# Kernel optimization log

Measured on AMD Instinct MI355X. Metric: run time of the kernel, lower is better.

The kernel has to match this reference:

```python
import jax, jax.numpy as jnp
import numpy as np

N, P, D, LM, NQ = 128, 576, 1536, 4096, 64
ALPHA, FPQ, TEMP, LR_G, EPS = 0.5, 14, 0.5, 0.1, 1e-20
NUM_CUBES = max(round(N / FPQ) - 1, 1)  # static: 8


def setup_inputs() -> dict:
    key = jax.random.key(0)
    ks = jax.random.split(key, 10)
    s = 1.0 / np.sqrt(D)
    return {
        "video_features": jax.random.normal(ks[0], (N, P, D), jnp.float32),
        "gumbel_u": jax.random.uniform(ks[1], (N - 1, 2), jnp.float32),
        "W_agg": jax.random.normal(ks[2], (D, D), jnp.float32) * s,
        "b_agg": jnp.zeros((D,), jnp.float32),
        "ln_g": jnp.ones((D,), jnp.float32),
        "ln_b": jnp.zeros((D,), jnp.float32),
        "W1": jax.random.normal(ks[3], (D, D), jnp.float32) * s,
        "b1": jnp.zeros((D,), jnp.float32),
        "W2": jax.random.normal(ks[4], (D, 2), jnp.float32) * s,
        "b2": jnp.zeros((2,), jnp.float32),
        "W_th": jax.random.normal(ks[5], (D, LM), jnp.float32) * s,
        "b_th": jnp.zeros((LM,), jnp.float32),
    }


def _forward(video_features, gumbel_u, W_agg, b_agg, ln_g, ln_b, W1, b1, W2, b2, W_th, b_th):
    # Step 1: momentum EMA over frame diffs: delta_1 = d_1; delta_i = a*d_i + (1-a)*delta_{i-1}
    diffs = video_features[1:] - video_features[:-1]            # [N-1, P, D]
    def step(carry, d):
        new = ALPHA * d + (1.0 - ALPHA) * carry
        return new, new
    _, rest = jax.lax.scan(step, diffs[0], diffs[1:])
    mom = jnp.concatenate([diffs[:1], rest], axis=0)            # [N-1, P, D]
    # Step 2: aggregate momentum features, mean over patches
    agg = jnp.einsum('npd,de->npe', mom, W_agg) + b_agg
    feat = agg.mean(axis=1)                                     # [N-1, D]
    # Step 3: gate network (LayerNorm -> Linear -> GELU -> Linear)
    mu = feat.mean(-1, keepdims=True)
    var = ((feat - mu) ** 2).mean(-1, keepdims=True)
    xn = (feat - mu) / jnp.sqrt(var + 1e-5) * ln_g + ln_b
    h = jax.nn.gelu(xn @ W1 + b1, approximate=False)
    gate_logits = h @ W2 + b2                                   # [N-1, 2]
    # Step 4: straight-through Gumbel-Softmax top-k
    g = -jnp.log(-jnp.log(gumbel_u + EPS) + EPS)
    y = jax.nn.softmax((gate_logits + g * LR_G) / TEMP, axis=-1)[:, 1]  # [N-1]
    _, ind = jax.lax.top_k(y, NUM_CUBES)
    y_hard = jnp.zeros_like(y).at[ind].set(1.0)
    z_hard = jax.lax.stop_gradient(y_hard - y) + y
    # Step 5: force first frame as keyframe
    z_hard = jnp.concatenate([jnp.ones((1,), z_hard.dtype), z_hard], axis=0)  # [N]
    # Step 7: thumbnail = keyframe-weighted mean -> adaptive avg pool (576->64) -> Linear
    tf = jnp.einsum('n,npd->pd', z_hard, video_features) / z_hard.sum()  # [P, D]
    pooled = tf.reshape(NQ, P // NQ, D).mean(axis=1)                     # [NQ, D]
    thumbnail = pooled @ W_th + b_th                                     # [NQ, LM]
    return gate_logits, thumbnail, z_hard


def reference(video_features, gumbel_u, W_agg, b_agg, ln_g, ln_b, W1, b1, W2, b2, W_th, b_th):
    return _forward(video_features, gumbel_u, W_agg, b_agg, ln_g, ln_b, W1, b1, W2, b2, W_th, b_th)
```

## Files before the change

### kernel.cpp

```cpp
#include <hip/hip_runtime.h>

#define NFR   128
#define PP    576
#define DD    1536
#define LMM   4096
#define NQQ   64
#define PQ    9
#define NCUBES 8
#define NSEL  9
#define D4    384

#define OFF_A      0u
#define OFF_VFMEAN 1572864u
#define OFF_MOM    1769472u
#define OFF_XN     1966080u
#define OFF_H      2162688u
#define OFF_PPART  2359296u
#define OFF_POOLED 3244032u
#define OFF_Y      3342336u
#define OFF_SEL    3342464u

#define OUT_GATE  0
#define OUT_THUMB 254
#define OUT_Z     262398

__global__ __launch_bounds__(384) void k1_partial(const float* __restrict__ vf,
                                                  float* __restrict__ part) {
    const int n  = blockIdx.x;
    const int ps = blockIdx.y;
    const int c4 = threadIdx.x;
    const float4* v = (const float4*)vf;
    float4 acc = make_float4(0.f, 0.f, 0.f, 0.f);
    int base = (n * PP + ps * 72) * D4 + c4;
#pragma unroll 8
    for (int p = 0; p < 72; ++p) {
        float4 x = v[base + p * D4];
        acc.x += x.x; acc.y += x.y; acc.z += x.z; acc.w += x.w;
    }
    ((float4*)part)[(n * 8 + ps) * D4 + c4] = acc;
}

__global__ __launch_bounds__(256) void k2a_mean(const float* __restrict__ part,
                                                float* __restrict__ vfMean) {
    const int n = blockIdx.x;
    const int d = blockIdx.y * 256 + threadIdx.x;
    float s = 0.f;
#pragma unroll
    for (int ps = 0; ps < 8; ++ps) s += part[(n * 8 + ps) * DD + d];
    vfMean[n * DD + d] = s * (1.0f / 576.0f);
}

__global__ __launch_bounds__(256) void k2b_scan(const float* __restrict__ vfMean,
                                                float* __restrict__ momMean) {
    const int d = blockIdx.x * 256 + threadIdx.x;
    float prev = vfMean[d];
    float cur  = vfMean[DD + d];
    float ema  = cur - prev;
    momMean[d] = ema;
    prev = cur;
    for (int n = 2; n < NFR; ++n) {
        cur = vfMean[n * DD + d];
        float diff = cur - prev;
        ema = 0.5f * diff + 0.5f * ema;
        momMean[(n - 1) * DD + d] = ema;
        prev = cur;
    }
    momMean[127 * DD + d] = 0.f;
}

#define GKC 16
__global__ __launch_bounds__(256) void gemm_sk(const float* __restrict__ A,
                                               const float* __restrict__ B,
                                               float* __restrict__ Cpart,
                                               int M, int N, int K, int kChunk) {
    const int j0 = blockIdx.x * 64;
    const int i0 = blockIdx.y * 64;
    const int s  = blockIdx.z;
    const int k0 = s * kChunk;
    __shared__ float As[GKC][68];
    __shared__ float Bs[GKC][68];
    const int tid = threadIdx.x;
    const int tx = tid & 15, ty = tid >> 4;
    const int ai = tid >> 2, ak4 = (tid & 3) * 4;
    const int bk = tid >> 4, bj4 = (tid & 15) * 4;
    float c[4][4] = {};
    for (int kk = k0; kk < k0 + kChunk; kk += GKC) {
        float4 av = *(const float4*)(A + (size_t)(i0 + ai) * K + kk + ak4);
        float4 bv = *(const float4*)(B + (size_t)(kk + bk) * N + j0 + bj4);
        __syncthreads();
        As[ak4 + 0][ai] = av.x; As[ak4 + 1][ai] = av.y;
        As[ak4 + 2][ai] = av.z; As[ak4 + 3][ai] = av.w;
        Bs[bk][bj4 + 0] = bv.x; Bs[bk][bj4 + 1] = bv.y;
        Bs[bk][bj4 + 2] = bv.z; Bs[bk][bj4 + 3] = bv.w;
        __syncthreads();
#pragma unroll
        for (int k = 0; k < GKC; ++k) {
            float a0 = As[k][ty * 4 + 0], a1 = As[k][ty * 4 + 1];
            float a2 = As[k][ty * 4 + 2], a3 = As[k][ty * 4 + 3];
            float b0 = Bs[k][tx * 4 + 0], b1 = Bs[k][tx * 4 + 1];
            float b2 = Bs[k][tx * 4 + 2], b3 = Bs[k][tx * 4 + 3];
            c[0][0] += a0 * b0; c[0][1] += a0 * b1; c[0][2] += a0 * b2; c[0][3] += a0 * b3;
            c[1][0] += a1 * b0; c[1][1] += a1 * b1; c[1][2] += a1 * b2; c[1][3] += a1 * b3;
            c[2][0] += a2 * b0; c[2][1] += a2 * b1; c[2][2] += a2 * b2; c[2][3] += a2 * b3;
            c[3][0] += a3 * b0; c[3][1] += a3 * b1; c[3][2] += a3 * b2; c[3][3] += a3 * b3;
        }
    }
    float* Cp = Cpart + (size_t)s * M * N;
#pragma unroll
    for (int ii = 0; ii < 4; ++ii)
#pragma unroll
        for (int jj = 0; jj < 4; ++jj)
            Cp[(size_t)(i0 + ty * 4 + ii) * N + j0 + tx * 4 + jj] = c[ii][jj];
}

__device__ __forceinline__ float blockSum(float v, float* sb) {
#pragma unroll
    for (int o = 32; o > 0; o >>= 1) v += __shfl_down(v, o);
    __syncthreads();
    if ((threadIdx.x & 63) == 0) sb[threadIdx.x >> 6] = v;
    __syncthreads();
    return sb[0] + sb[1] + sb[2] + sb[3];
}

__global__ __launch_bounds__(256) void k4_ln(const float* __restrict__ Cpart,
                                             const float* __restrict__ b_agg,
                                             const float* __restrict__ ln_g,
                                             const float* __restrict__ ln_b,
                                             float* __restrict__ xn) {
    __shared__ float sb[4];
    const int n = blockIdx.x;
    if (n == 127) {
#pragma unroll
        for (int t = 0; t < 6; ++t) xn[n * DD + t * 256 + threadIdx.x] = 0.f;
        return;
    }
    float v[6];
#pragma unroll
    for (int t = 0; t < 6; ++t) {
        int d = t * 256 + threadIdx.x;
        float s = b_agg[d];
#pragma unroll
        for (int ss = 0; ss < 8; ++ss) s += Cpart[ss * (NFR * DD) + n * DD + d];
        v[t] = s;
    }
    float local = v[0] + v[1] + v[2] + v[3] + v[4] + v[5];
    float mu = blockSum(local, sb) * (1.0f / (float)DD);
    float ls = 0.f;
#pragma unroll
    for (int t = 0; t < 6; ++t) { float dd = v[t] - mu; ls += dd * dd; }
    float var = blockSum(ls, sb) * (1.0f / (float)DD);
    float rstd = rsqrtf(var + 1e-5f);
#pragma unroll
    for (int t = 0; t < 6; ++t) {
        int d = t * 256 + threadIdx.x;
        xn[n * DD + d] = (v[t] - mu) * rstd * ln_g[d] + ln_b[d];
    }
}

__global__ __launch_bounds__(256) void k5b_gelu(const float* __restrict__ Cpart,
                                                const float* __restrict__ b1,
                                                float* __restrict__ h) {
    const int n = blockIdx.x;
    const int d = blockIdx.y * 256 + threadIdx.x;
    float s = b1[d];
#pragma unroll
    for (int ss = 0; ss < 8; ++ss) s += Cpart[ss * (NFR * DD) + n * DD + d];
    h[n * DD + d] = 0.5f * s * (1.0f + erff(s * 0.70710678118654752f));
}

__global__ __launch_bounds__(256) void k6_gate(const float* __restrict__ h,
                                               const float* __restrict__ W2,
                                               const float* __restrict__ b2,
                                               const float* __restrict__ u,
                                               float* __restrict__ outGate,
                                               float* __restrict__ y) {
    __shared__ float sb[4];
    const int n = blockIdx.x;
    float a0 = 0.f, a1 = 0.f;
#pragma unroll
    for (int t = 0; t < 6; ++t) {
        int d = t * 256 + threadIdx.x;
        float hv = h[n * DD + d];
        a0 += hv * W2[2 * d];
        a1 += hv * W2[2 * d + 1];
    }
    a0 = blockSum(a0, sb);
    a1 = blockSum(a1, sb);
    if (threadIdx.x == 0) {
        float gl0 = a0 + b2[0], gl1 = a1 + b2[1];
        outGate[2 * n]     = gl0;
        outGate[2 * n + 1] = gl1;
        float g0 = -logf(-logf(u[2 * n]     + 1e-20f) + 1e-20f);
        float g1 = -logf(-logf(u[2 * n + 1] + 1e-20f) + 1e-20f);
        float s0 = (gl0 + g0 * 0.1f) * 2.0f;
        float s1 = (gl1 + g1 * 0.1f) * 2.0f;
        float m = fmaxf(s0, s1);
        float e0 = expf(s0 - m), e1 = expf(s1 - m);
        y[n] = e1 / (e0 + e1);
    }
}

__global__ __launch_bounds__(64) void k7_topk(const float* __restrict__ y,
                                              int* __restrict__ selFrames,
                                              float* __restrict__ outZ) {
    __shared__ float yv[127];
    __shared__ int   tk[127];
    const int t = threadIdx.x;
    for (int i = t; i < 127; i += 64) { yv[i] = y[i]; tk[i] = 0; }
    __syncthreads();
    if (t == 0) {
        selFrames[0] = 0;
        for (int c = 0; c < NCUBES; ++c) {
            float best = -1e30f; int bi = 0;
            for (int i = 0; i < 127; ++i)
                if (!tk[i] && yv[i] > best) { best = yv[i]; bi = i; }
            tk[bi] = 1;
            selFrames[c + 1] = bi + 1;
        }
        outZ[0] = 1.0f;
        for (int i = 0; i < 127; ++i)
            outZ[1 + i] = tk[i] ? 1.0f : 0.0f;
    }
}

__global__ __launch_bounds__(384) void k8_pool(const float* __restrict__ vf,
                                               const int* __restrict__ selFrames,
                                               float* __restrict__ pPart) {
    const int q = blockIdx.x, slot = blockIdx.y, c4 = threadIdx.x;
    const int n = selFrames[slot];
    const float4* v = (const float4*)vf;
    float4 acc = make_float4(0.f, 0.f, 0.f, 0.f);
    int base = (n * PP + q * PQ) * D4 + c4;
#pragma unroll
    for (int r = 0; r < PQ; ++r) {
        float4 x = v[base + r * D4];
        acc.x += x.x; acc.y += x.y; acc.z += x.z; acc.w += x.w;
    }
    ((float4*)pPart)[(slot * NQQ + q) * D4 + c4] = acc;
}

__global__ __launch_bounds__(256) void k8b_pool(const float* __restrict__ pPart,
                                                float* __restrict__ pooled) {
    const int q = blockIdx.x;
    const int d = blockIdx.y * 256 + threadIdx.x;
    float s = 0.f;
#pragma unroll
    for (int slot = 0; slot < NSEL; ++slot) s += pPart[(slot * NQQ + q) * DD + d];
    pooled[q * DD + d] = s * (1.0f / 81.0f);
}

__global__ __launch_bounds__(256) void k10_thumb(const float* __restrict__ Cpart,
                                                 const float* __restrict__ b_th,
                                                 float* __restrict__ outT) {
    const int q = blockIdx.x;
    const int l = blockIdx.y * 256 + threadIdx.x;
    float s = b_th[l];
#pragma unroll
    for (int ss = 0; ss < 4; ++ss) s += Cpart[ss * (NQQ * LMM) + q * LMM + l];
    outT[q * LMM + l] = s;
}

extern "C" void kernel_launch(void* const* d_in, const int* in_sizes, int n_in,
                              void* d_out, int out_size, void* d_ws, size_t ws_size,
                              hipStream_t stream) {
    const float* vf    = (const float*)d_in[0];
    const float* u     = (const float*)d_in[1];
    const float* W_agg = (const float*)d_in[2];
    const float* b_agg = (const float*)d_in[3];
    const float* ln_g  = (const float*)d_in[4];
    const float* ln_b  = (const float*)d_in[5];
    const float* W1    = (const float*)d_in[6];
    const float* b1    = (const float*)d_in[7];
    const float* W2    = (const float*)d_in[8];
    const float* b2    = (const float*)d_in[9];
    const float* W_th  = (const float*)d_in[10];
    const float* b_th  = (const float*)d_in[11];

    float* ws = (float*)d_ws;
    float* regA    = ws + OFF_A;
    float* vfMean  = ws + OFF_VFMEAN;
    float* momMean = ws + OFF_MOM;
    float* xn      = ws + OFF_XN;
    float* h       = ws + OFF_H;
    float* pPart   = ws + OFF_PPART;
    float* pooled  = ws + OFF_POOLED;
    float* yv      = ws + OFF_Y;
    int*   sel     = (int*)(ws + OFF_SEL);

    float* out = (float*)d_out;
    float* outGate  = out + OUT_GATE;
    float* outThumb = out + OUT_THUMB;
    float* outZ     = out + OUT_Z;

    k1_partial<<<dim3(NFR, 8), 384, 0, stream>>>(vf, regA);
    k2a_mean<<<dim3(NFR, 6), 256, 0, stream>>>(regA, vfMean);
    k2b_scan<<<6, 256, 0, stream>>>(vfMean, momMean);
    gemm_sk<<<dim3(24, 2, 8), 256, 0, stream>>>(momMean, W_agg, regA, NFR, DD, DD, 192);
    k4_ln<<<NFR, 256, 0, stream>>>(regA, b_agg, ln_g, ln_b, xn);
    gemm_sk<<<dim3(24, 2, 8), 256, 0, stream>>>(xn, W1, regA, NFR, DD, DD, 192);
    k5b_gelu<<<dim3(127, 6), 256, 0, stream>>>(regA, b1, h);
    k6_gate<<<127, 256, 0, stream>>>(h, W2, b2, u, outGate, yv);
    k7_topk<<<1, 64, 0, stream>>>(yv, sel, outZ);
    k8_pool<<<dim3(NQQ, NSEL), 384, 0, stream>>>(vf, sel, pPart);
    k8b_pool<<<dim3(NQQ, 6), 256, 0, stream>>>(pPart, pooled);
    gemm_sk<<<dim3(64, 1, 4), 256, 0, stream>>>(pooled, W_th, regA, NQQ, LMM, DD, 384);
    k10_thumb<<<dim3(NQQ, 16), 256, 0, stream>>>(regA, b_th, outThumb);
}
```

Before: 813.5 us.

## Fuse mean into scan, GELU into gate, prefetch GEMM tiles, parallelize top-k

```diff
diff --git a/kernel.cpp b/kernel.cpp
--- a/kernel.cpp
+++ b/kernel.cpp
@@ -40,26 +40,24 @@
     ((float4*)part)[(n * 8 + ps) * D4 + c4] = acc;
 }
 
-__global__ __launch_bounds__(256) void k2a_mean(const float* __restrict__ part,
-                                                float* __restrict__ vfMean) {
-    const int n = blockIdx.x;
-    const int d = blockIdx.y * 256 + threadIdx.x;
+__device__ __forceinline__ float frameMean(const float* __restrict__ part, int n, int d) {
     float s = 0.f;
 #pragma unroll
     for (int ps = 0; ps < 8; ++ps) s += part[(n * 8 + ps) * DD + d];
-    vfMean[n * DD + d] = s * (1.0f / 576.0f);
-}
-
-__global__ __launch_bounds__(256) void k2b_scan(const float* __restrict__ vfMean,
-                                                float* __restrict__ momMean) {
-    const int d = blockIdx.x * 256 + threadIdx.x;
-    float prev = vfMean[d];
-    float cur  = vfMean[DD + d];
+    return s * (1.0f / 576.0f);
+}
+
+__global__ __launch_bounds__(64) void k2_scan(const float* __restrict__ part,
+                                              float* __restrict__ momMean) {
+    const int d = blockIdx.x * 64 + threadIdx.x;
+    float prev = frameMean(part, 0, d);
+    float cur  = frameMean(part, 1, d);
     float ema  = cur - prev;
     momMean[d] = ema;
     prev = cur;
+#pragma unroll 4
     for (int n = 2; n < NFR; ++n) {
-        cur = vfMean[n * DD + d];
+        cur = frameMean(part, n, d);
         float diff = cur - prev;
         ema = 0.5f * diff + 0.5f * ema;
         momMean[(n - 1) * DD + d] = ema;
@@ -84,15 +82,21 @@
     const int ai = tid >> 2, ak4 = (tid & 3) * 4;
     const int bk = tid >> 4, bj4 = (tid & 15) * 4;
     float c[4][4] = {};
+    const float* Ap = A + (size_t)(i0 + ai) * K + ak4;
+    const float* Bp = B + (size_t)bk * N + j0 + bj4;
+    float4 av = *(const float4*)(Ap + k0);
+    float4 bv = *(const float4*)(Bp + (size_t)k0 * N);
     for (int kk = k0; kk < k0 + kChunk; kk += GKC) {
-        float4 av = *(const float4*)(A + (size_t)(i0 + ai) * K + kk + ak4);
-        float4 bv = *(const float4*)(B + (size_t)(kk + bk) * N + j0 + bj4);
         __syncthreads();
         As[ak4 + 0][ai] = av.x; As[ak4 + 1][ai] = av.y;
         As[ak4 + 2][ai] = av.z; As[ak4 + 3][ai] = av.w;
         Bs[bk][bj4 + 0] = bv.x; Bs[bk][bj4 + 1] = bv.y;
         Bs[bk][bj4 + 2] = bv.z; Bs[bk][bj4 + 3] = bv.w;
         __syncthreads();
+        if (kk + GKC < k0 + kChunk) {
+            av = *(const float4*)(Ap + kk + GKC);
+            bv = *(const float4*)(Bp + (size_t)(kk + GKC) * N);
+        }
 #pragma unroll
         for (int k = 0; k < GKC; ++k) {
             float a0 = As[k][ty * 4 + 0], a1 = As[k][ty * 4 + 1];
@@ -157,18 +161,8 @@
     }
 }
 
-__global__ __launch_bounds__(256) void k5b_gelu(const float* __restrict__ Cpart,
-                                                const float* __restrict__ b1,
-                                                float* __restrict__ h) {
-    const int n = blockIdx.x;
-    const int d = blockIdx.y * 256 + threadIdx.x;
-    float s = b1[d];
-#pragma unroll
-    for (int ss = 0; ss < 8; ++ss) s += Cpart[ss * (NFR * DD) + n * DD + d];
-    h[n * DD + d] = 0.5f * s * (1.0f + erff(s * 0.70710678118654752f));
-}
-
-__global__ __launch_bounds__(256) void k6_gate(const float* __restrict__ h,
+__global__ __launch_bounds__(256) void k6_gate(const float* __restrict__ Cpart,
+                                               const float* __restrict__ b1,
                                                const float* __restrict__ W2,
                                                const float* __restrict__ b2,
                                                const float* __restrict__ u,
@@ -180,7 +174,10 @@
 #pragma unroll
     for (int t = 0; t < 6; ++t) {
         int d = t * 256 + threadIdx.x;
-        float hv = h[n * DD + d];
+        float s = b1[d];
+#pragma unroll
+        for (int ss = 0; ss < 8; ++ss) s += Cpart[ss * (NFR * DD) + n * DD + d];
+        float hv = 0.5f * s * (1.0f + erff(s * 0.70710678118654752f));
         a0 += hv * W2[2 * d];
         a1 += hv * W2[2 * d + 1];
     }
@@ -200,27 +197,37 @@
     }
 }
 
-__global__ __launch_bounds__(64) void k7_topk(const float* __restrict__ y,
-                                              int* __restrict__ selFrames,
-                                              float* __restrict__ outZ) {
-    __shared__ float yv[127];
-    __shared__ int   tk[127];
+__global__ __launch_bounds__(128) void k7_topk(const float* __restrict__ y,
+                                               int* __restrict__ selFrames,
+                                               float* __restrict__ outZ) {
+    __shared__ float vals[128];
+    __shared__ int   taken[128];
+    __shared__ float wv[2];
+    __shared__ int   wi[2];
     const int t = threadIdx.x;
-    for (int i = t; i < 127; i += 64) { yv[i] = y[i]; tk[i] = 0; }
+    vals[t]  = (t < 127) ? y[t] : -1e30f;
+    taken[t] = 0;
     __syncthreads();
-    if (t == 0) {
-        selFrames[0] = 0;
-        for (int c = 0; c < NCUBES; ++c) {
-            float best = -1e30f; int bi = 0;
-            for (int i = 0; i < 127; ++i)
-                if (!tk[i] && yv[i] > best) { best = yv[i]; bi = i; }
-            tk[bi] = 1;
-            selFrames[c + 1] = bi + 1;
+    for (int c = 0; c < NCUBES; ++c) {
+        float v = taken[t] ? -1e30f : vals[t];
+        int   i = t;
+#pragma unroll
+        for (int o = 32; o > 0; o >>= 1) {
+            float ov = __shfl_down(v, o);
+            int   oi = __shfl_down(i, o);
+            if (ov > v || (ov == v && oi < i)) { v = ov; i = oi; }
         }
-        outZ[0] = 1.0f;
-        for (int i = 0; i < 127; ++i)
-            outZ[1 + i] = tk[i] ? 1.0f : 0.0f;
-    }
+        if ((t & 63) == 0) { wv[t >> 6] = v; wi[t >> 6] = i; }
+        __syncthreads();
+        if (t == 0) {
+            int win = (wv[1] > wv[0] || (wv[1] == wv[0] && wi[1] < wi[0])) ? wi[1] : wi[0];
+            taken[win] = 1;
+            selFrames[c + 1] = win + 1;
+        }
+        __syncthreads();
+    }
+    if (t == 0) { selFrames[0] = 0; outZ[0] = 1.0f; }
+    if (t < 127) outZ[1 + t] = taken[t] ? 1.0f : 0.0f;
 }
 
 __global__ __launch_bounds__(384) void k8_pool(const float* __restrict__ vf,
@@ -278,10 +285,8 @@
 
     float* ws = (float*)d_ws;
     float* regA    = ws + OFF_A;
-    float* vfMean  = ws + OFF_VFMEAN;
     float* momMean = ws + OFF_MOM;
     float* xn      = ws + OFF_XN;
-    float* h       = ws + OFF_H;
     float* pPart   = ws + OFF_PPART;
     float* pooled  = ws + OFF_POOLED;
     float* yv      = ws + OFF_Y;
@@ -293,14 +298,12 @@
     float* outZ     = out + OUT_Z;
 
     k1_partial<<<dim3(NFR, 8), 384, 0, stream>>>(vf, regA);
-    k2a_mean<<<dim3(NFR, 6), 256, 0, stream>>>(regA, vfMean);
-    k2b_scan<<<6, 256, 0, stream>>>(vfMean, momMean);
+    k2_scan<<<24, 64, 0, stream>>>(regA, momMean);
     gemm_sk<<<dim3(24, 2, 8), 256, 0, stream>>>(momMean, W_agg, regA, NFR, DD, DD, 192);
     k4_ln<<<NFR, 256, 0, stream>>>(regA, b_agg, ln_g, ln_b, xn);
     gemm_sk<<<dim3(24, 2, 8), 256, 0, stream>>>(xn, W1, regA, NFR, DD, DD, 192);
-    k5b_gelu<<<dim3(127, 6), 256, 0, stream>>>(regA, b1, h);
-    k6_gate<<<127, 256, 0, stream>>>(h, W2, b2, u, outGate, yv);
-    k7_topk<<<1, 64, 0, stream>>>(yv, sel, outZ);
+    k6_gate<<<127, 256, 0, stream>>>(regA, b1, W2, b2, u, outGate, yv);
+    k7_topk<<<1, 128, 0, stream>>>(yv, sel, outZ);
     k8_pool<<<dim3(NQQ, NSEL), 384, 0, stream>>>(vf, sel, pPart);
     k8b_pool<<<dim3(NQQ, 6), 256, 0, stream>>>(pPart, pooled);
     gemm_sk<<<dim3(64, 1, 4), 256, 0, stream>>>(pooled, W_th, regA, NQQ, LMM, DD, 384);
```

Measured after the change: 733.1 us. -9.9%, faster.
